# Kernel tuning notes

Hardware: AMD Instinct MI355X
Metric: run time of the kernel (lower is better)

The kernel has to match this reference:

```python
import jax, jax.numpy as jnp
import numpy as np

N_HEADS = 16
NEG_INF = float('-inf')


def setup_inputs() -> dict:
    key = jax.random.key(0)
    ks = jax.random.split(key, 8)
    B, S, D = 8, 1024, 1024
    inp = {
        'q': jax.random.normal(ks[0], (B, S, D), jnp.float32),
        'k': jax.random.normal(ks[1], (B, S, D), jnp.float32),
        'v': jax.random.normal(ks[2], (B, S, D), jnp.float32),
        'key_padding_mask': jnp.zeros((B, S), bool),
        'Wq': jax.random.normal(ks[3], (D, D), jnp.float32) / np.sqrt(D),
        'bq': jnp.zeros((D,), jnp.float32),
        'Wk': jax.random.normal(ks[4], (D, D), jnp.float32) / np.sqrt(D),
        'bk': jnp.zeros((D,), jnp.float32),
        'Wv': jax.random.normal(ks[5], (D, D), jnp.float32) / np.sqrt(D),
        'bv': jnp.zeros((D,), jnp.float32),
        'Wo': jax.random.normal(ks[6], (D, D), jnp.float32) / np.sqrt(D),
        'bo': jnp.zeros((D,), jnp.float32),
    }
    return inp


def reference(q, k, v, key_padding_mask, Wq, bq, Wk, bk, Wv, bv, Wo, bo):
    B, T, D = q.shape
    S = k.shape[1]
    H = N_HEADS
    dh = D // H
    causal = True

    # projections (torch Linear: x @ W.T + b)
    qh = (q @ Wq.T + bq).reshape(B, T, H, dh).transpose(0, 2, 1, 3)  # b h t d
    kh = (k @ Wk.T + bk).reshape(B, S, H, dh).transpose(0, 2, 1, 3)  # b h s d
    vh = (v @ Wv.T + bv).reshape(B, S, H, dh).transpose(0, 2, 1, 3)  # b h s d

    s = jnp.einsum('bhtd,bhsd->bhts', qh, kh) / jnp.sqrt(jnp.asarray(dh, s_dtype(qh)))
    s = jnp.where(key_padding_mask[:, None, None, :], NEG_INF, s)
    if causal:
        cmask = jnp.triu(jnp.full((T, S), NEG_INF, s.dtype), 1)
        s = s + cmask[None, None]
    a = jax.nn.softmax(s.astype(jnp.float32), axis=-1).astype(s.dtype)
    o = jnp.einsum('bhts,bhsd->bhtd', a, vh)
    o = o.transpose(0, 2, 1, 3).reshape(B, T, D)
    return o @ Wo.T + bo


def s_dtype(x):
    return x.dtype
```

## Files before the change

### kernel.cpp

```cpp
#include <hip/hip_runtime.h>
#include <hip/hip_bf16.h>

typedef unsigned short u16;
typedef unsigned int u32;
typedef __attribute__((ext_vector_type(8))) short bf16x8;
typedef __attribute__((ext_vector_type(4))) float f32x4;
typedef __attribute__((ext_vector_type(4))) unsigned int u32x4v;

#define LOG2E 1.44269504088896340736f
#define QSCALE (0.125f * LOG2E)


__device__ inline u16 f2bf(float f) {
  union { float f; u32 u; } v; v.f = f;
  u32 r = v.u + 0x7fffu + ((v.u >> 16) & 1u);
  return (u16)(r >> 16);
}

__device__ inline void gload_lds16(const void* g, void* l) {
  __builtin_amdgcn_global_load_lds(
      (const __attribute__((address_space(1))) u32*)g,
      (__attribute__((address_space(3))) u32*)l, 16, 0, 0);
}

template<int CTRL>
__device__ inline float dppmov(float x) {
  int i = __builtin_bit_cast(int, x);
  int r = __builtin_amdgcn_update_dpp(i, i, CTRL, 0xf, 0xf, false);
  return __builtin_bit_cast(float, r);
}
__device__ inline float rowmax16(float v) {
  v = fmaxf(v, dppmov<0x128>(v));
  v = fmaxf(v, dppmov<0x124>(v));
  v = fmaxf(v, dppmov<0x122>(v));
  v = fmaxf(v, dppmov<0x121>(v));
  return v;
}
__device__ inline float rowsum16(float v) {
  v += dppmov<0x128>(v);
  v += dppmov<0x124>(v);
  v += dppmov<0x122>(v);
  v += dppmov<0x121>(v);
  return v;
}


__global__ void cvt_multi(const float4* __restrict__ s0, const float4* __restrict__ s1,
                          const float4* __restrict__ s2, const float4* __restrict__ s3,
                          ushort4* __restrict__ d0, ushort4* __restrict__ d1,
                          ushort4* __restrict__ d2, ushort4* __restrict__ d3, int n4) {
  const float4* s; ushort4* d;
  switch (blockIdx.y) {
    case 0: s = s0; d = d0; break;
    case 1: s = s1; d = d1; break;
    case 2: s = s2; d = d2; break;
    default: s = s3; d = d3; break;
  }
  int stride = gridDim.x * blockDim.x;
  for (int i = blockIdx.x * blockDim.x + threadIdx.x; i < n4; i += stride) {
    float4 v = s[i];
    ushort4 o;
    o.x = f2bf(v.x); o.y = f2bf(v.y); o.z = f2bf(v.z); o.w = f2bf(v.w);
    d[i] = o;
  }
}


__global__ void mask_flags(const unsigned char* __restrict__ mask,
                           unsigned char* __restrict__ flags) {
  int t = threadIdx.x;
  if (t >= 128) return;
  const uint4* p = (const uint4*)(mask + (size_t)t * 64);
  uint4 a = p[0], b = p[1], c = p[2], d = p[3];
  u32 v = a.x | a.y | a.z | a.w | b.x | b.y | b.z | b.w |
          c.x | c.y | c.z | c.w | d.x | d.y | d.z | d.w;
  flags[t] = v ? 1 : 0;
}


__global__ __launch_bounds__(256) void gemm_qkv_f32a(
    const float* __restrict__ Aqf, const float* __restrict__ Akf, const float* __restrict__ Avf,
    const u16* __restrict__ Wqb, const u16* __restrict__ Wkb, const u16* __restrict__ Wvb,
    const float* __restrict__ bqp, const float* __restrict__ bkp, const float* __restrict__ bvp,
    u16* __restrict__ Qh, u16* __restrict__ Kh, u16* __restrict__ Vt,
    int M, int N, int K) {
  constexpr int BK = 32;
  __shared__ float sAf[2][128 * BK];
  __shared__ u16   sB [2][128 * BK];

  const int nx = gridDim.x;
  const int nxy = gridDim.x * gridDim.y;
  const int nwg = nxy * gridDim.z;
  const int hw = blockIdx.z * nxy + blockIdx.y * nx + blockIdx.x;
  const int per = nwg >> 3;
  const int lg = (hw & 7) * per + (hw >> 3);
  const int z = lg / nxy;
  const int rem = lg - z * nxy;
  const int m0 = (rem >> 3) * 128;
  const int n0 = (rem & 7) * 128;

  const float* Af = (z == 0) ? Aqf : (z == 1) ? Akf : Avf;
  const u16* Bt   = (z == 0) ? Wqb : (z == 1) ? Wkb : Wvb;
  const float* bias = (z == 0) ? bqp : (z == 1) ? bkp : bvp;

  const int tid = threadIdx.x;
  const int lane = tid & 63;
  const int wave = tid >> 6;
  const int g = lane >> 4;
  const int r = lane & 15;
  const int wr = wave >> 1, wc = wave & 1;

  f32x4 acc[4][4] = {};

  auto stage = [&](int buf, int kt) {
    const int k0 = kt * BK;
#pragma unroll
    for (int i = 0; i < 4; ++i) {
      int c = tid + i * 256;
      int row = c >> 3, cc = c & 7;
      int scc = cc ^ (row & 7);
      gload_lds16(Af + (size_t)(m0 + row) * K + k0 + scc * 4,
                  (char*)&sAf[buf][0] + c * 16);
    }
#pragma unroll
    for (int i = 0; i < 2; ++i) {
      int c = tid + i * 256;
      int row = c >> 2, cc = c & 3;
      int scc = cc ^ ((row >> 1) & 3);
      gload_lds16(Bt + (size_t)(n0 + row) * K + k0 + scc * 8,
                  (char*)&sB[buf][0] + c * 16);
    }
  };

  auto compute = [&](int buf) {
    const char* aB = (const char*)&sAf[buf][0];
    const char* bB = (const char*)&sB[buf][0];
    bf16x8 avf[4], bvf[4];
#pragma unroll
    for (int i = 0; i < 4; ++i) {
      int arow = wr * 64 + i * 16 + r;
      const char* rb = aB + arow * 128;
      int s7 = arow & 7;
      uint4 q0 = *(const uint4*)(rb + (((g * 2)     ^ s7) * 16));
      uint4 q1 = *(const uint4*)(rb + (((g * 2 + 1) ^ s7) * 16));
      u32x4v w;
      w.x = __builtin_amdgcn_perm(q0.y, q0.x, 0x07060302u);
      w.y = __builtin_amdgcn_perm(q0.w, q0.z, 0x07060302u);
      w.z = __builtin_amdgcn_perm(q1.y, q1.x, 0x07060302u);
      w.w = __builtin_amdgcn_perm(q1.w, q1.z, 0x07060302u);
      avf[i] = __builtin_bit_cast(bf16x8, w);
      int brow = wc * 64 + i * 16 + r;
      bvf[i] = *(const bf16x8*)(bB + brow * 64 + ((g ^ ((brow >> 1) & 3)) * 16));
    }
#pragma unroll
    for (int i = 0; i < 4; ++i)
#pragma unroll
      for (int j = 0; j < 4; ++j)
        acc[i][j] = __builtin_amdgcn_mfma_f32_16x16x32_bf16(avf[i], bvf[j], acc[i][j], 0, 0, 0);
  };

  stage(0, 0);
  const int NT = K / BK;
  for (int kt = 0; kt < NT; ++kt) {
    __syncthreads();
    if (kt + 1 < NT) stage((kt + 1) & 1, kt + 1);
    compute(kt & 1);
  }

#pragma unroll
  for (int i = 0; i < 4; ++i) {
    int rowb = m0 + wr * 64 + i * 16 + g * 4;
#pragma unroll
    for (int j = 0; j < 4; ++j) {
      int col = n0 + wc * 64 + j * 16 + r;
      float bv = bias[col];
#pragma unroll
      for (int q = 0; q < 4; ++q) {
        int row = rowb + q;
        float v = acc[i][j][q] + bv;
        int b = row >> 10, t = row & 1023, h = col >> 6, d = col & 63;
        if (z == 0) {
          Qh[((((size_t)b * 16 + h) << 10) + t) * 64 + d] = f2bf(v * QSCALE);
        } else if (z == 1) {
          Kh[((((size_t)b * 16 + h) << 10) + t) * 64 + d] = f2bf(v);
        } else {
          Vt[(((size_t)b * 16 + h) * 64 + d) * 1024 + t] = f2bf(v);
        }
      }
    }
  }
}


__global__ __launch_bounds__(256) void gemm_o(
    const u16* __restrict__ A, const u16* __restrict__ Bt,
    const float* __restrict__ bias, float* __restrict__ Cout,
    int M, int N, int K) {
  constexpr int BK = 32;
  __shared__ u16 sA[2][128 * BK];
  __shared__ u16 sB[2][128 * BK];

  const int nx = gridDim.x;
  const int nwg = gridDim.x * gridDim.y;
  const int hw = blockIdx.y * nx + blockIdx.x;
  const int per = nwg >> 3;
  const int lg = (hw & 7) * per + (hw >> 3);
  const int m0 = (lg >> 3) * 128;
  const int n0 = (lg & 7) * 128;

  const int tid = threadIdx.x;
  const int lane = tid & 63;
  const int wave = tid >> 6;
  const int g = lane >> 4;
  const int r = lane & 15;
  const int wr = wave >> 1, wc = wave & 1;

  f32x4 acc[4][4] = {};

  auto stage = [&](int buf, int kt) {
    const int k0 = kt * BK;
#pragma unroll
    for (int i = 0; i < 2; ++i) {
      int c = tid + i * 256;
      int row = c >> 2, cc = c & 3;
      int scc = cc ^ ((row >> 1) & 3);
      gload_lds16(A + (size_t)(m0 + row) * K + k0 + scc * 8,
                  (char*)&sA[buf][0] + c * 16);
    }
#pragma unroll
    for (int i = 0; i < 2; ++i) {
      int c = tid + i * 256;
      int row = c >> 2, cc = c & 3;
      int scc = cc ^ ((row >> 1) & 3);
      gload_lds16(Bt + (size_t)(n0 + row) * K + k0 + scc * 8,
                  (char*)&sB[buf][0] + c * 16);
    }
  };

  stage(0, 0);
  const int NT = K / BK;
  for (int kt = 0; kt < NT; ++kt) {
    __syncthreads();
    if (kt + 1 < NT) stage((kt + 1) & 1, kt + 1);
    const char* aB = (const char*)&sA[kt & 1][0];
    const char* bB = (const char*)&sB[kt & 1][0];
    bf16x8 avf[4], bvf[4];
#pragma unroll
    for (int i = 0; i < 4; ++i) {
      int arow = wr * 64 + i * 16 + r;
      avf[i] = *(const bf16x8*)(aB + arow * 64 + ((g ^ ((arow >> 1) & 3)) * 16));
      int brow = wc * 64 + i * 16 + r;
      bvf[i] = *(const bf16x8*)(bB + brow * 64 + ((g ^ ((brow >> 1) & 3)) * 16));
    }
#pragma unroll
    for (int i = 0; i < 4; ++i)
#pragma unroll
      for (int j = 0; j < 4; ++j)
        acc[i][j] = __builtin_amdgcn_mfma_f32_16x16x32_bf16(avf[i], bvf[j], acc[i][j], 0, 0, 0);
  }

#pragma unroll
  for (int i = 0; i < 4; ++i) {
    int rowb = m0 + wr * 64 + i * 16 + g * 4;
#pragma unroll
    for (int j = 0; j < 4; ++j) {
      int col = n0 + wc * 64 + j * 16 + r;
      float bv = bias[col];
#pragma unroll
      for (int q = 0; q < 4; ++q) {
        int row = rowb + q;
        Cout[(size_t)row * N + col] = acc[i][j][q] + bv;
      }
    }
  }
}


__global__ __launch_bounds__(256) void attn_fwd(
    const u16* __restrict__ Qh, const u16* __restrict__ Kh,
    const u16* __restrict__ Vt, const unsigned char* __restrict__ mask,
    const unsigned char* __restrict__ padflags,
    u16* __restrict__ O) {
  constexpr int S = 1024, DH = 64;
  __shared__ u16 sK[2][64 * 64];
  __shared__ u16 sV[2][64 * 64];
  __shared__ u16 sP[4][16 * 64];

  const int tid = threadIdx.x, lane = tid & 63, wave = tid >> 6;
  const int g = lane >> 4, r = lane & 15;
  const int bh = blockIdx.x;
  const int qt = (int)gridDim.y - 1 - (int)blockIdx.y;
  const int b = bh >> 4, h = bh & 15;
  const int qw = qt * 128 + wave * 32;

  bf16x8 qf[2][2];
#pragma unroll
  for (int u = 0; u < 2; ++u) {
    const u16* Qb = Qh + ((size_t)bh * S + qw + u * 16 + r) * DH;
    qf[u][0] = *(const bf16x8*)(Qb + g * 8);
    qf[u][1] = *(const bf16x8*)(Qb + 32 + g * 8);
  }

  f32x4 acc[2][4] = {};
  float mrun[2][4], lrun[2][4];
#pragma unroll
  for (int u = 0; u < 2; ++u)
#pragma unroll
    for (int i = 0; i < 4; ++i) { mrun[u][i] = -INFINITY; lrun[u][i] = 0.f; }

  auto stage = [&](int buf, int kvt) {
    const int s0k = kvt * 64;
#pragma unroll
    for (int i = 0; i < 2; ++i) {
      int c = tid + i * 256;
      int row = c >> 3;
      int cc = (c & 7) ^ (row & 7);
      gload_lds16(Kh + ((size_t)bh * S + s0k + row) * DH + cc * 8, &sK[buf][0] + c * 8);
      gload_lds16(Vt + ((size_t)bh * DH + row) * S + s0k + cc * 8, &sV[buf][0] + c * 8);
    }
  };

  const int NT = 2 * (qt + 1);
  stage(0, 0);
  for (int kvt = 0; kvt < NT; ++kvt) {
    __syncthreads();
    if (kvt + 1 < NT) stage((kvt + 1) & 1, kvt + 1);
    const int cur = kvt & 1;
    const int s0 = kvt * 64;
    const bool pad = padflags[b * 16 + (s0 >> 6)] != 0;
    const u16* Kb = &sK[cur][0];
    const u16* Vb = &sV[cur][0];
    u16* Pw = &sP[wave][0];

#pragma unroll
    for (int u = 0; u < 2; ++u) {
      const int qg = qw + u * 16;
      if (s0 > qg + 15) continue;
      const bool diag = (s0 + 63 > qg);

      f32x4 sc[4] = {};
#pragma unroll
      for (int ss = 0; ss < 4; ++ss) {
#pragma unroll
        for (int kc = 0; kc < 2; ++kc) {
          int krow = ss * 16 + r;
          int byteoff = krow * 128 + kc * 64 + g * 16;
          bf16x8 kf = *(const bf16x8*)((const char*)Kb + (byteoff ^ ((krow & 7) << 4)));
          sc[ss] = __builtin_amdgcn_mfma_f32_16x16x32_bf16(qf[u][kc], kf, sc[ss], 0, 0, 0);
        }
      }

      float sv[4][4];
      float pmax[4] = {-INFINITY, -INFINITY, -INFINITY, -INFINITY};
#pragma unroll
      for (int ss = 0; ss < 4; ++ss) {
        float padd = 0.f;
        if (pad) {
          int s_g = s0 + ss * 16 + r;
          if (mask[(size_t)b * S + s_g]) padd = -INFINITY;
        }
#pragma unroll
        for (int reg = 0; reg < 4; ++reg) {
          float v = sc[ss][reg] + padd;
          if (diag) {
            int s_g = s0 + ss * 16 + r;
            int q_g = qg + g * 4 + reg;
            if (s_g > q_g) v = -INFINITY;
          }
          sv[ss][reg] = v;
          pmax[reg] = fmaxf(pmax[reg], v);
        }
      }
#pragma unroll
      for (int reg = 0; reg < 4; ++reg) {
        float m = rowmax16(pmax[reg]);
        float newm = fmaxf(mrun[u][reg], m);
        float alpha = (newm == -INFINITY) ? 1.f : exp2f(mrun[u][reg] - newm);
        mrun[u][reg] = newm;
        float rs = 0.f;
#pragma unroll
        for (int ss = 0; ss < 4; ++ss) {
          float p = (newm == -INFINITY) ? 0.f : exp2f(sv[ss][reg] - newm);
          sv[ss][reg] = p;
          rs += p;
        }
        rs = rowsum16(rs);
        lrun[u][reg] = lrun[u][reg] * alpha + rs;
#pragma unroll
        for (int df = 0; df < 4; ++df) acc[u][df][reg] *= alpha;
      }

#pragma unroll
      for (int ss = 0; ss < 4; ++ss) {
#pragma unroll
        for (int reg = 0; reg < 4; ++reg) {
          int qrow = g * 4 + reg;
          int byteoff = qrow * 128 + (ss * 16 + r) * 2;
          u32 bits = __builtin_bit_cast(u32, sv[ss][reg]);
          *(u16*)((char*)Pw + (byteoff ^ ((qrow & 7) << 4))) = (u16)(bits >> 16);
        }
      }

#pragma unroll
      for (int sc2 = 0; sc2 < 2; ++sc2) {
        int pbyte = r * 128 + sc2 * 64 + g * 16;
        bf16x8 pf = *(const bf16x8*)((const char*)Pw + (pbyte ^ ((r & 7) << 4)));
#pragma unroll
        for (int df = 0; df < 4; ++df) {
          int vrow = df * 16 + r;
          int vbyte = vrow * 128 + sc2 * 64 + g * 16;
          bf16x8 vf = *(const bf16x8*)((const char*)Vb + (vbyte ^ ((vrow & 7) << 4)));
          acc[u][df] = __builtin_amdgcn_mfma_f32_16x16x32_bf16(pf, vf, acc[u][df], 0, 0, 0);
        }
      }
    }
  }

#pragma unroll
  for (int u = 0; u < 2; ++u) {
#pragma unroll
    for (int reg = 0; reg < 4; ++reg) {
      float l = lrun[u][reg];
      float inv = (l > 0.f) ? 1.f / l : 0.f;
      int t = qw + u * 16 + g * 4 + reg;
#pragma unroll
      for (int df = 0; df < 4; ++df) {
        float vo = acc[u][df][reg] * inv;
        O[((size_t)b * 1024 + t) * 1024 + h * 64 + df * 16 + r] = f2bf(vo);
      }
    }
  }
}


extern "C" void kernel_launch(void* const* d_in, const int* in_sizes, int n_in,
                              void* d_out, int out_size, void* d_ws, size_t ws_size,
                              hipStream_t stream) {
  const float* q  = (const float*)d_in[0];
  const float* k  = (const float*)d_in[1];
  const float* v  = (const float*)d_in[2];
  const unsigned char* mask = (const unsigned char*)d_in[3];
  const float* Wq = (const float*)d_in[4];
  const float* bq = (const float*)d_in[5];
  const float* Wk = (const float*)d_in[6];
  const float* bk = (const float*)d_in[7];
  const float* Wv = (const float*)d_in[8];
  const float* bv = (const float*)d_in[9];
  const float* Wo = (const float*)d_in[10];
  const float* bo = (const float*)d_in[11];

  const int M = 8192, N = 1024, K = 1024;
  const size_t MB = 1u << 20;
  char* ws = (char*)d_ws;

  u16* AttO = (u16*)(ws);
  u16* Qh   = (u16*)(ws + 16 * MB);
  u16* Kh   = (u16*)(ws + 32 * MB);
  u16* Vt   = (u16*)(ws + 48 * MB);
  u16* Wqb  = (u16*)(ws + 64 * MB);
  u16* Wkb  = Wqb + (1u << 20);
  u16* Wvb  = Wkb + (1u << 20);
  u16* Wob  = Wvb + (1u << 20);
  unsigned char* flags = (unsigned char*)(ws + 72 * MB);

  cvt_multi<<<dim3(256, 4), 256, 0, stream>>>(
      (const float4*)Wq, (const float4*)Wk, (const float4*)Wv, (const float4*)Wo,
      (ushort4*)Wqb, (ushort4*)Wkb, (ushort4*)Wvb, (ushort4*)Wob, (N * K) / 4);
  mask_flags<<<1, 128, 0, stream>>>(mask, flags);

  gemm_qkv_f32a<<<dim3(N / 128, M / 128, 3), 256, 0, stream>>>(
      q, k, v, Wqb, Wkb, Wvb, bq, bk, bv, Qh, Kh, Vt, M, N, K);

  attn_fwd<<<dim3(128, 8), 256, 0, stream>>>(Qh, Kh, Vt, mask, flags, AttO);

  gemm_o<<<dim3(N / 128, M / 128), 256, 0, stream>>>(
      AttO, Wob, bo, (float*)d_out, M, N, K);
}
```

Baseline: 216.5 us.

## Triple-buffer GEMM LDS staging with vmcnt waits and drop B-tile swizzle

Both projection GEMMs move from double-buffered LDS staging with __syncthreads to a three-stage ring. Loads for tile kt+2 are issued before computing tile kt, and explicit s_waitcnt vmcnt plus s_barrier replace the full sync so two tiles of global loads stay in flight. The XOR swizzle on bf16 tiles is removed in favour of plain row-major LDS addressing, which may add bank conflicts on the fragment reads. LDS use grows by half, which can lower occupancy.

```diff
diff --git a/kernel.cpp b/kernel.cpp
--- a/kernel.cpp
+++ b/kernel.cpp
@@ -22,6 +22,8 @@
       (const __attribute__((address_space(1))) u32*)g,
       (__attribute__((address_space(3))) u32*)l, 16, 0, 0);
 }
+
+#define WAITCNT_VM(N) asm volatile("s_waitcnt vmcnt(" #N ")" ::: "memory")
 
 template<int CTRL>
 __device__ inline float dppmov(float x) {
@@ -85,8 +87,8 @@
     u16* __restrict__ Qh, u16* __restrict__ Kh, u16* __restrict__ Vt,
     int M, int N, int K) {
   constexpr int BK = 32;
-  __shared__ float sAf[2][128 * BK];
-  __shared__ u16   sB [2][128 * BK];
+  __shared__ float sAf[3][128 * BK];
+  __shared__ u16   sB [3][128 * BK];
 
   const int nx = gridDim.x;
   const int nxy = gridDim.x * gridDim.y;
@@ -126,8 +128,7 @@
     for (int i = 0; i < 2; ++i) {
       int c = tid + i * 256;
       int row = c >> 2, cc = c & 3;
-      int scc = cc ^ ((row >> 1) & 3);
-      gload_lds16(Bt + (size_t)(n0 + row) * K + k0 + scc * 8,
+      gload_lds16(Bt + (size_t)(n0 + row) * K + k0 + cc * 8,
                   (char*)&sB[buf][0] + c * 16);
     }
   };
@@ -150,7 +151,7 @@
       w.w = __builtin_amdgcn_perm(q1.w, q1.z, 0x07060302u);
       avf[i] = __builtin_bit_cast(bf16x8, w);
       int brow = wc * 64 + i * 16 + r;
-      bvf[i] = *(const bf16x8*)(bB + brow * 64 + ((g ^ ((brow >> 1) & 3)) * 16));
+      bvf[i] = *(const bf16x8*)(bB + brow * 64 + g * 16);
     }
 #pragma unroll
     for (int i = 0; i < 4; ++i)
@@ -159,12 +160,29 @@
         acc[i][j] = __builtin_amdgcn_mfma_f32_16x16x32_bf16(avf[i], bvf[j], acc[i][j], 0, 0, 0);
   };
 
+  const int NT = K / BK;
+
   stage(0, 0);
-  const int NT = K / BK;
+  stage(1, 1);
+  WAITCNT_VM(6);
+  __builtin_amdgcn_s_barrier();
+
+  int cb = 0;
   for (int kt = 0; kt < NT; ++kt) {
-    __syncthreads();
-    if (kt + 1 < NT) stage((kt + 1) & 1, kt + 1);
-    compute(kt & 1);
+    if (kt + 2 < NT) {
+      int b2 = cb + 2; if (b2 >= 3) b2 -= 3;
+      stage(b2, kt + 2);
+      compute(cb);
+      WAITCNT_VM(6);
+      __builtin_amdgcn_s_barrier();
+    } else if (kt + 1 < NT) {
+      compute(cb);
+      WAITCNT_VM(0);
+      __builtin_amdgcn_s_barrier();
+    } else {
+      compute(cb);
+    }
+    cb = (cb == 2) ? 0 : cb + 1;
   }
 
 #pragma unroll
@@ -197,8 +215,8 @@
     const float* __restrict__ bias, float* __restrict__ Cout,
     int M, int N, int K) {
   constexpr int BK = 32;
-  __shared__ u16 sA[2][128 * BK];
-  __shared__ u16 sB[2][128 * BK];
+  __shared__ u16 sA[3][128 * BK];
+  __shared__ u16 sB[3][128 * BK];
 
   const int nx = gridDim.x;
   const int nwg = gridDim.x * gridDim.y;
@@ -223,40 +241,57 @@
     for (int i = 0; i < 2; ++i) {
       int c = tid + i * 256;
       int row = c >> 2, cc = c & 3;
-      int scc = cc ^ ((row >> 1) & 3);
-      gload_lds16(A + (size_t)(m0 + row) * K + k0 + scc * 8,
+      gload_lds16(A + (size_t)(m0 + row) * K + k0 + cc * 8,
                   (char*)&sA[buf][0] + c * 16);
     }
 #pragma unroll
     for (int i = 0; i < 2; ++i) {
       int c = tid + i * 256;
       int row = c >> 2, cc = c & 3;
-      int scc = cc ^ ((row >> 1) & 3);
-      gload_lds16(Bt + (size_t)(n0 + row) * K + k0 + scc * 8,
+      gload_lds16(Bt + (size_t)(n0 + row) * K + k0 + cc * 8,
                   (char*)&sB[buf][0] + c * 16);
     }
   };
 
-  stage(0, 0);
-  const int NT = K / BK;
-  for (int kt = 0; kt < NT; ++kt) {
-    __syncthreads();
-    if (kt + 1 < NT) stage((kt + 1) & 1, kt + 1);
-    const char* aB = (const char*)&sA[kt & 1][0];
-    const char* bB = (const char*)&sB[kt & 1][0];
+  auto compute = [&](int buf) {
+    const u16* aB = &sA[buf][0];
+    const u16* bB = &sB[buf][0];
     bf16x8 avf[4], bvf[4];
 #pragma unroll
     for (int i = 0; i < 4; ++i) {
-      int arow = wr * 64 + i * 16 + r;
-      avf[i] = *(const bf16x8*)(aB + arow * 64 + ((g ^ ((arow >> 1) & 3)) * 16));
-      int brow = wc * 64 + i * 16 + r;
-      bvf[i] = *(const bf16x8*)(bB + brow * 64 + ((g ^ ((brow >> 1) & 3)) * 16));
+      avf[i] = *(const bf16x8*)(aB + (wr * 64 + i * 16 + r) * BK + g * 8);
+      bvf[i] = *(const bf16x8*)(bB + (wc * 64 + i * 16 + r) * BK + g * 8);
     }
 #pragma unroll
     for (int i = 0; i < 4; ++i)
 #pragma unroll
       for (int j = 0; j < 4; ++j)
         acc[i][j] = __builtin_amdgcn_mfma_f32_16x16x32_bf16(avf[i], bvf[j], acc[i][j], 0, 0, 0);
+  };
+
+  const int NT = K / BK;
+
+  stage(0, 0);
+  stage(1, 1);
+  WAITCNT_VM(4);
+  __builtin_amdgcn_s_barrier();
+
+  int cb = 0;
+  for (int kt = 0; kt < NT; ++kt) {
+    if (kt + 2 < NT) {
+      int b2 = cb + 2; if (b2 >= 3) b2 -= 3;
+      stage(b2, kt + 2);
+      compute(cb);
+      WAITCNT_VM(4);
+      __builtin_amdgcn_s_barrier();
+    } else if (kt + 1 < NT) {
+      compute(cb);
+      WAITCNT_VM(0);
+      __builtin_amdgcn_s_barrier();
+    } else {
+      compute(cb);
+    }
+    cb = (cb == 2) ? 0 : cb + 1;
   }
 
 #pragma unroll
```

New measurement: 271.7 us. 1.26x slower.

## Pre-convert activations to bf16 and use 256x128 tiles with 512-thread GEMMs

Applied to the files above, without the earlier changes.

Adds a separate pass that converts the fp32 q/k/v activations to bf16 in the workspace, so the QKV GEMM loads bf16 A tiles directly instead of staging fp32 and packing in registers. Both GEMMs move to 256x128 output tiles with 512 threads (8 waves), which halves the grid and raises reuse of each B tile. The XOR swizzle on LDS staging is dropped, which may bring back LDS bank conflicts. The extra conversion pass costs additional global memory traffic.

```diff
diff --git a/kernel.cpp b/kernel.cpp
--- a/kernel.cpp
+++ b/kernel.cpp
@@ -5,7 +5,6 @@
 typedef unsigned int u32;
 typedef __attribute__((ext_vector_type(8))) short bf16x8;
 typedef __attribute__((ext_vector_type(4))) float f32x4;
-typedef __attribute__((ext_vector_type(4))) unsigned int u32x4v;
 
 #define LOG2E 1.44269504088896340736f
 #define QSCALE (0.125f * LOG2E)
@@ -78,29 +77,28 @@
 }
 
 
-__global__ __launch_bounds__(256) void gemm_qkv_f32a(
-    const float* __restrict__ Aqf, const float* __restrict__ Akf, const float* __restrict__ Avf,
+__global__ __launch_bounds__(512) void gemm_qkv(
+    const u16* __restrict__ Aq, const u16* __restrict__ Ak, const u16* __restrict__ Av,
     const u16* __restrict__ Wqb, const u16* __restrict__ Wkb, const u16* __restrict__ Wvb,
     const float* __restrict__ bqp, const float* __restrict__ bkp, const float* __restrict__ bvp,
     u16* __restrict__ Qh, u16* __restrict__ Kh, u16* __restrict__ Vt,
     int M, int N, int K) {
   constexpr int BK = 32;
-  __shared__ float sAf[2][128 * BK];
-  __shared__ u16   sB [2][128 * BK];
-
-  const int nx = gridDim.x;
+  __shared__ u16 sA[2][256 * BK];
+  __shared__ u16 sB[2][128 * BK];
+
   const int nxy = gridDim.x * gridDim.y;
   const int nwg = nxy * gridDim.z;
-  const int hw = blockIdx.z * nxy + blockIdx.y * nx + blockIdx.x;
+  const int hw = blockIdx.z * nxy + blockIdx.y * gridDim.x + blockIdx.x;
   const int per = nwg >> 3;
   const int lg = (hw & 7) * per + (hw >> 3);
-  const int z = lg / nxy;
-  const int rem = lg - z * nxy;
-  const int m0 = (rem >> 3) * 128;
+  const int z = lg >> 8;
+  const int rem = lg & 255;
+  const int m0 = (rem >> 3) * 256;
   const int n0 = (rem & 7) * 128;
 
-  const float* Af = (z == 0) ? Aqf : (z == 1) ? Akf : Avf;
-  const u16* Bt   = (z == 0) ? Wqb : (z == 1) ? Wkb : Wvb;
+  const u16* A  = (z == 0) ? Aq : (z == 1) ? Ak : Av;
+  const u16* Bt = (z == 0) ? Wqb : (z == 1) ? Wkb : Wvb;
   const float* bias = (z == 0) ? bqp : (z == 1) ? bkp : bvp;
 
   const int tid = threadIdx.x;
@@ -108,49 +106,34 @@
   const int wave = tid >> 6;
   const int g = lane >> 4;
   const int r = lane & 15;
-  const int wr = wave >> 1, wc = wave & 1;
+  const int wr = wave >> 1;
+  const int wc = wave & 1;
 
   f32x4 acc[4][4] = {};
 
   auto stage = [&](int buf, int kt) {
     const int k0 = kt * BK;
 #pragma unroll
+    for (int i = 0; i < 2; ++i) {
+      int c = tid + i * 512;
+      int row = c >> 2, cc = c & 3;
+      gload_lds16(A + (size_t)(m0 + row) * K + k0 + cc * 8, &sA[buf][0] + c * 8);
+    }
+    {
+      int c = tid;
+      int row = c >> 2, cc = c & 3;
+      gload_lds16(Bt + (size_t)(n0 + row) * K + k0 + cc * 8, &sB[buf][0] + c * 8);
+    }
+  };
+
+  auto compute = [&](int buf) {
+    const u16* aB = &sA[buf][0];
+    const u16* bB = &sB[buf][0];
+    bf16x8 avf[4], bvf[4];
+#pragma unroll
     for (int i = 0; i < 4; ++i) {
-      int c = tid + i * 256;
-      int row = c >> 3, cc = c & 7;
-      int scc = cc ^ (row & 7);
-      gload_lds16(Af + (size_t)(m0 + row) * K + k0 + scc * 4,
-                  (char*)&sAf[buf][0] + c * 16);
-    }
-#pragma unroll
-    for (int i = 0; i < 2; ++i) {
-      int c = tid + i * 256;
-      int row = c >> 2, cc = c & 3;
-      int scc = cc ^ ((row >> 1) & 3);
-      gload_lds16(Bt + (size_t)(n0 + row) * K + k0 + scc * 8,
-                  (char*)&sB[buf][0] + c * 16);
-    }
-  };
-
-  auto compute = [&](int buf) {
-    const char* aB = (const char*)&sAf[buf][0];
-    const char* bB = (const char*)&sB[buf][0];
-    bf16x8 avf[4], bvf[4];
-#pragma unroll
-    for (int i = 0; i < 4; ++i) {
-      int arow = wr * 64 + i * 16 + r;
-      const char* rb = aB + arow * 128;
-      int s7 = arow & 7;
-      uint4 q0 = *(const uint4*)(rb + (((g * 2)     ^ s7) * 16));
-      uint4 q1 = *(const uint4*)(rb + (((g * 2 + 1) ^ s7) * 16));
-      u32x4v w;
-      w.x = __builtin_amdgcn_perm(q0.y, q0.x, 0x07060302u);
-      w.y = __builtin_amdgcn_perm(q0.w, q0.z, 0x07060302u);
-      w.z = __builtin_amdgcn_perm(q1.y, q1.x, 0x07060302u);
-      w.w = __builtin_amdgcn_perm(q1.w, q1.z, 0x07060302u);
-      avf[i] = __builtin_bit_cast(bf16x8, w);
-      int brow = wc * 64 + i * 16 + r;
-      bvf[i] = *(const bf16x8*)(bB + brow * 64 + ((g ^ ((brow >> 1) & 3)) * 16));
+      avf[i] = *(const bf16x8*)(aB + (wr * 64 + i * 16 + r) * BK + g * 8);
+      bvf[i] = *(const bf16x8*)(bB + (wc * 64 + i * 16 + r) * BK + g * 8);
     }
 #pragma unroll
     for (int i = 0; i < 4; ++i)
@@ -192,20 +175,19 @@
 }
 
 
-__global__ __launch_bounds__(256) void gemm_o(
+__global__ __launch_bounds__(512) void gemm_o(
     const u16* __restrict__ A, const u16* __restrict__ Bt,
     const float* __restrict__ bias, float* __restrict__ Cout,
     int M, int N, int K) {
   constexpr int BK = 32;
-  __shared__ u16 sA[2][128 * BK];
+  __shared__ u16 sA[2][256 * BK];
   __shared__ u16 sB[2][128 * BK];
 
-  const int nx = gridDim.x;
   const int nwg = gridDim.x * gridDim.y;
-  const int hw = blockIdx.y * nx + blockIdx.x;
+  const int hw = blockIdx.y * gridDim.x + blockIdx.x;
   const int per = nwg >> 3;
   const int lg = (hw & 7) * per + (hw >> 3);
-  const int m0 = (lg >> 3) * 128;
+  const int m0 = (lg >> 3) * 256;
   const int n0 = (lg & 7) * 128;
 
   const int tid = threadIdx.x;
@@ -221,20 +203,31 @@
     const int k0 = kt * BK;
 #pragma unroll
     for (int i = 0; i < 2; ++i) {
-      int c = tid + i * 256;
+      int c = tid + i * 512;
       int row = c >> 2, cc = c & 3;
-      int scc = cc ^ ((row >> 1) & 3);
-      gload_lds16(A + (size_t)(m0 + row) * K + k0 + scc * 8,
-                  (char*)&sA[buf][0] + c * 16);
-    }
-#pragma unroll
-    for (int i = 0; i < 2; ++i) {
-      int c = tid + i * 256;
+      gload_lds16(A + (size_t)(m0 + row) * K + k0 + cc * 8, &sA[buf][0] + c * 8);
+    }
+    {
+      int c = tid;
       int row = c >> 2, cc = c & 3;
-      int scc = cc ^ ((row >> 1) & 3);
-      gload_lds16(Bt + (size_t)(n0 + row) * K + k0 + scc * 8,
-                  (char*)&sB[buf][0] + c * 16);
-    }
+      gload_lds16(Bt + (size_t)(n0 + row) * K + k0 + cc * 8, &sB[buf][0] + c * 8);
+    }
+  };
+
+  auto compute = [&](int buf) {
+    const u16* aB = &sA[buf][0];
+    const u16* bB = &sB[buf][0];
+    bf16x8 avf[4], bvf[4];
+#pragma unroll
+    for (int i = 0; i < 4; ++i) {
+      avf[i] = *(const bf16x8*)(aB + (wr * 64 + i * 16 + r) * BK + g * 8);
+      bvf[i] = *(const bf16x8*)(bB + (wc * 64 + i * 16 + r) * BK + g * 8);
+    }
+#pragma unroll
+    for (int i = 0; i < 4; ++i)
+#pragma unroll
+      for (int j = 0; j < 4; ++j)
+        acc[i][j] = __builtin_amdgcn_mfma_f32_16x16x32_bf16(avf[i], bvf[j], acc[i][j], 0, 0, 0);
   };
 
   stage(0, 0);
@@ -242,21 +235,7 @@
   for (int kt = 0; kt < NT; ++kt) {
     __syncthreads();
     if (kt + 1 < NT) stage((kt + 1) & 1, kt + 1);
-    const char* aB = (const char*)&sA[kt & 1][0];
-    const char* bB = (const char*)&sB[kt & 1][0];
-    bf16x8 avf[4], bvf[4];
-#pragma unroll
-    for (int i = 0; i < 4; ++i) {
-      int arow = wr * 64 + i * 16 + r;
-      avf[i] = *(const bf16x8*)(aB + arow * 64 + ((g ^ ((arow >> 1) & 3)) * 16));
-      int brow = wc * 64 + i * 16 + r;
-      bvf[i] = *(const bf16x8*)(bB + brow * 64 + ((g ^ ((brow >> 1) & 3)) * 16));
-    }
-#pragma unroll
-    for (int i = 0; i < 4; ++i)
-#pragma unroll
-      for (int j = 0; j < 4; ++j)
-        acc[i][j] = __builtin_amdgcn_mfma_f32_16x16x32_bf16(avf[i], bvf[j], acc[i][j], 0, 0, 0);
+    compute(kt & 1);
   }
 
 #pragma unroll
@@ -453,26 +432,32 @@
   const size_t MB = 1u << 20;
   char* ws = (char*)d_ws;
 
-  u16* AttO = (u16*)(ws);
-  u16* Qh   = (u16*)(ws + 16 * MB);
-  u16* Kh   = (u16*)(ws + 32 * MB);
-  u16* Vt   = (u16*)(ws + 48 * MB);
-  u16* Wqb  = (u16*)(ws + 64 * MB);
+  u16* Aq   = (u16*)(ws);
+  u16* Ak   = (u16*)(ws + 16 * MB);
+  u16* Av   = (u16*)(ws + 32 * MB);
+  u16* Qh   = (u16*)(ws + 48 * MB);
+  u16* Kh   = (u16*)(ws + 64 * MB);
+  u16* Vt   = (u16*)(ws + 80 * MB);
+  u16* Wqb  = (u16*)(ws + 96 * MB);
   u16* Wkb  = Wqb + (1u << 20);
   u16* Wvb  = Wkb + (1u << 20);
   u16* Wob  = Wvb + (1u << 20);
-  unsigned char* flags = (unsigned char*)(ws + 72 * MB);
-
+  unsigned char* flags = (unsigned char*)(ws + 104 * MB);
+  u16* AttO = Aq;
+
+  cvt_multi<<<dim3(1024, 3), 256, 0, stream>>>(
+      (const float4*)q, (const float4*)k, (const float4*)v, (const float4*)q,
+      (ushort4*)Aq, (ushort4*)Ak, (ushort4*)Av, (ushort4*)Aq, (M * K) / 4);
   cvt_multi<<<dim3(256, 4), 256, 0, stream>>>(
       (const float4*)Wq, (const float4*)Wk, (const float4*)Wv, (const float4*)Wo,
       (ushort4*)Wqb, (ushort4*)Wkb, (ushort4*)Wvb, (ushort4*)Wob, (N * K) / 4);
   mask_flags<<<1, 128, 0, stream>>>(mask, flags);
 
-  gemm_qkv_f32a<<<dim3(N / 128, M / 128, 3), 256, 0, stream>>>(
-      q, k, v, Wqb, Wkb, Wvb, bq, bk, bv, Qh, Kh, Vt, M, N, K);
+  gemm_qkv<<<dim3(8, 32, 3), 512, 0, stream>>>(
+      Aq, Ak, Av, Wqb, Wkb, Wvb, bq, bk, bv, Qh, Kh, Vt, M, N, K);
 
   attn_fwd<<<dim3(128, 8), 256, 0, stream>>>(Qh, Kh, Vt, mask, flags, AttO);
 
-  gemm_o<<<dim3(N / 128, M / 128), 256, 0, stream>>>(
+  gemm_o<<<dim3(8, 32), 512, 0, stream>>>(
       AttO, Wob, bo, (float*)d_out, M, N, K);
 }
```

Measured after the change: 239.0 us. 10.4% more time.
